# Kernel tuning notes

Measured on AMD Instinct MI355X. Metric: run time of the kernel, lower is better.

Reference implementation:

```python
import jax, jax.numpy as jnp
import numpy as np

B, N, C = 2, 8192, 768
H, K = 12, 256
D = C // H
HID = 4 * C
EPS = 1e-6

def layer_norm(x, w, b):
    mu = jnp.mean(x, axis=-1, keepdims=True)
    var = jnp.mean(jnp.square(x - mu), axis=-1, keepdims=True)
    return (x - mu) * jax.lax.rsqrt(var + EPS) * w + b

def setup_inputs() -> dict:
    key = jax.random.key(0)
    ks = jax.random.split(key, 8)
    s = 0.02
    return {
        "x": jax.random.normal(ks[0], (B, N, C), jnp.float32),
        "ln1_w": jnp.ones((C,), jnp.float32),
        "ln1_b": jnp.zeros((C,), jnp.float32),
        "qkv_w": jax.random.normal(ks[1], (C, 3 * C), jnp.float32) * s,
        "qkv_b": jnp.zeros((3 * C,), jnp.float32),
        "Ek": jax.random.normal(ks[2], (N, K), jnp.float32) * s,
        "Ev": jax.random.normal(ks[3], (N, K), jnp.float32) * s,
        "proj_w": jax.random.normal(ks[4], (C, C), jnp.float32) * s,
        "proj_b": jnp.zeros((C,), jnp.float32),
        "ln2_w": jnp.ones((C,), jnp.float32),
        "ln2_b": jnp.zeros((C,), jnp.float32),
        "fc1_w": jax.random.normal(ks[5], (C, HID), jnp.float32) * s,
        "fc1_b": jnp.zeros((HID,), jnp.float32),
        "fc2_w": jax.random.normal(ks[6], (HID, C), jnp.float32) * s,
        "fc2_b": jnp.zeros((C,), jnp.float32),
    }

def reference(x, ln1_w, ln1_b, qkv_w, qkv_b, Ek, Ev, proj_w, proj_b,
              ln2_w, ln2_b, fc1_w, fc1_b, fc2_w, fc2_b):
    scale = D ** -0.5
    # --- attention branch ---
    h = layer_norm(x, ln1_w, ln1_b)
    qkv = h @ qkv_w + qkv_b                      # (B,N,3C)
    qkv = qkv.reshape(B, N, 3, H, D).transpose(2, 0, 3, 1, 4)  # (3,B,H,N,D)
    q, k, v = qkv[0], qkv[1], qkv[2]
    # Linformer: project K/V along sequence dim N -> K
    k_proj = jnp.einsum('bhnd,nk->bhkd', k, Ek)
    v_proj = jnp.einsum('bhnd,nk->bhkd', v, Ev)
    logits = jnp.einsum('bhnd,bhkd->bhnk', q, k_proj) * scale
    logits = jnp.clip(logits, -50.0, 50.0)
    attn = jax.nn.softmax(logits, axis=-1)
    o = jnp.einsum('bhnk,bhkd->bhnd', attn, v_proj)
    o = o.transpose(0, 2, 1, 3).reshape(B, N, C)
    o = o @ proj_w + proj_b
    x = x + o                                    # alpha_attn = 1.0
    # --- MLP branch ---
    h = layer_norm(x, ln2_w, ln2_b)
    h = jax.nn.gelu(h @ fc1_w + fc1_b, approximate=False)
    h = h @ fc2_w + fc2_b
    return x + h                                 # alpha_mlp = 1.0
```

## Files before the change

kernel.cpp:

```cpp
#include <hip/hip_runtime.h>
#include <cstdint>

#define DEV __device__ __forceinline__

typedef __bf16 bf16x8 __attribute__((ext_vector_type(8)));
typedef float f32x4 __attribute__((ext_vector_type(4)));

DEV uint16_t f2bf(float f) {
  uint32_t u = __float_as_uint(f);
  u += 0x7FFFu + ((u >> 16) & 1u);
  return (uint16_t)(u >> 16);
}
DEV float bf2f(uint16_t h) { return __uint_as_float(((uint32_t)h) << 16); }

DEV void gload16(const void* g, void* l) {
  __builtin_amdgcn_global_load_lds((const __attribute__((address_space(1))) void*)g,
                                   (__attribute__((address_space(3))) void*)l, 16, 0, 0);
}

template <int N> DEV void waitcnt_vm() {
  if constexpr (N == 0) asm volatile("s_waitcnt vmcnt(0)" ::: "memory");
  else if constexpr (N == 3) asm volatile("s_waitcnt vmcnt(3)" ::: "memory");
  else if constexpr (N == 4) asm volatile("s_waitcnt vmcnt(4)" ::: "memory");
  else static_assert(N == 0 || N == 3 || N == 4, "unsupported vmcnt");
}

__global__ __launch_bounds__(256) void ln768(const float* __restrict__ x,
                                             const float* __restrict__ w,
                                             const float* __restrict__ b,
                                             uint16_t* __restrict__ out) {
  const size_t row = blockIdx.x;
  const float* xr = x + row * 768;
  const int t = threadIdx.x;
  float v0 = xr[t], v1 = xr[t + 256], v2 = xr[t + 512];
  float s = v0 + v1 + v2;
  float s2 = v0 * v0 + v1 * v1 + v2 * v2;
#pragma unroll
  for (int o = 32; o; o >>= 1) {
    s += __shfl_down(s, o);
    s2 += __shfl_down(s2, o);
  }
  __shared__ float sh[8];
  if ((t & 63) == 0) { sh[t >> 6] = s; sh[4 + (t >> 6)] = s2; }
  __syncthreads();
  s = sh[0] + sh[1] + sh[2] + sh[3];
  s2 = sh[4] + sh[5] + sh[6] + sh[7];
  const float mu = s * (1.f / 768.f);
  const float var = s2 * (1.f / 768.f) - mu * mu;
  const float rstd = rsqrtf(var + 1e-6f);
  uint16_t* orow = out + row * 768;
  orow[t]       = f2bf((v0 - mu) * rstd * w[t] + b[t]);
  orow[t + 256] = f2bf((v1 - mu) * rstd * w[t + 256] + b[t + 256]);
  orow[t + 512] = f2bf((v2 - mu) * rstd * w[t + 512] + b[t + 512]);
}

__global__ __launch_bounds__(256) void transpose_f2b(const float* __restrict__ in,
                                                     uint16_t* __restrict__ outp,
                                                     int ldin, int ldout) {
  __shared__ float tile[32][33];
  const int tx = threadIdx.x, ty = threadIdx.y;
  const size_t x = (size_t)blockIdx.x * 32 + tx;
  const size_t y = (size_t)blockIdx.y * 32 + ty;
#pragma unroll
  for (int j = 0; j < 4; ++j) tile[ty + j * 8][tx] = in[(y + j * 8) * ldin + x];
  __syncthreads();
  const size_t x2 = (size_t)blockIdx.y * 32 + tx;
  const size_t y2 = (size_t)blockIdx.x * 32 + ty;
#pragma unroll
  for (int j = 0; j < 4; ++j) outp[(y2 + j * 8) * ldout + x2] = f2bf(tile[tx][ty + j * 8]);
}

__global__ __launch_bounds__(256) void transpose_b2b(const uint16_t* __restrict__ in,
                                                     uint16_t* __restrict__ outp,
                                                     int ldin, int ldout) {
  __shared__ uint16_t tile[32][33];
  const int tx = threadIdx.x, ty = threadIdx.y;
  const size_t x = (size_t)blockIdx.x * 32 + tx;
  const size_t y = (size_t)blockIdx.y * 32 + ty;
#pragma unroll
  for (int j = 0; j < 4; ++j) tile[ty + j * 8][tx] = in[(y + j * 8) * ldin + x];
  __syncthreads();
  const size_t x2 = (size_t)blockIdx.y * 32 + tx;
  const size_t y2 = (size_t)blockIdx.x * 32 + ty;
#pragma unroll
  for (int j = 0; j < 4; ++j) outp[(y2 + j * 8) * ldout + x2] = tile[tx][ty + j * 8];
}

template <int BM, int BN, bool OUTBF, bool HASBIAS, bool DOGELU, bool HASRES>
__global__ __launch_bounds__(256) void gemm_nt(
    const uint16_t* __restrict__ Abase, const uint16_t* __restrict__ Bbase,
    void* __restrict__ Cbase, const float* __restrict__ bias,
    const float* __restrict__ resbase, int Kd, int lda, int ldb, int ldc,
    int zdiv, size_t sAhi, size_t sAlo, size_t sBhi, size_t sBlo,
    size_t sChi, size_t sClo) {
  const int z = blockIdx.z;
  const int zhi = z / zdiv, zlo = z - zhi * zdiv;
  const uint16_t* A = Abase + zhi * sAhi + zlo * sAlo;
  const uint16_t* B = Bbase + zhi * sBhi + zlo * sBlo;
  const size_t coff = zhi * sChi + zlo * sClo;

  constexpr int WTM = BM / 2, WTN = BN / 2;
  constexpr int FM = WTM / 16, FN = WTN / 16;
  const int tid = threadIdx.x;
  const int wave = tid >> 6, lane = tid & 63;
  const int wm = wave >> 1, wn = wave & 1;
  const int l16 = lane & 15, lhi = lane >> 4;

  __shared__ __align__(16) uint16_t sA[BM * 32];
  __shared__ __align__(16) uint16_t sB[BN * 32];

  f32x4 acc[FM][FN];
#pragma unroll
  for (int m = 0; m < FM; ++m)
#pragma unroll
    for (int n = 0; n < FN; ++n) acc[m][n] = f32x4{0.f, 0.f, 0.f, 0.f};

  const int row0 = blockIdx.x * BM;
  const int col0 = blockIdx.y * BN;
  const int rr = tid >> 2, cq = tid & 3;

  for (int k0 = 0; k0 < Kd; k0 += 32) {
    __syncthreads();
#pragma unroll
    for (int is = 0; is < BM / 64; ++is) {
      const uint16_t* g = A + (size_t)(row0 + is * 64 + rr) * lda + k0 + cq * 8;
      gload16(g, &sA[is * 2048 + tid * 8]);
    }
#pragma unroll
    for (int is = 0; is < BN / 64; ++is) {
      const uint16_t* g = B + (size_t)(col0 + is * 64 + rr) * ldb + k0 + cq * 8;
      gload16(g, &sB[is * 2048 + tid * 8]);
    }
    __syncthreads();

    bf16x8 af[FM], bq[FN];
#pragma unroll
    for (int m = 0; m < FM; ++m)
      af[m] = *(const bf16x8*)(&sA[(wm * WTM + m * 16 + l16) * 32 + lhi * 8]);
#pragma unroll
    for (int n = 0; n < FN; ++n)
      bq[n] = *(const bf16x8*)(&sB[(wn * WTN + n * 16 + l16) * 32 + lhi * 8]);
#pragma unroll
    for (int m = 0; m < FM; ++m)
#pragma unroll
      for (int n = 0; n < FN; ++n)
        acc[m][n] = __builtin_amdgcn_mfma_f32_16x16x32_bf16(af[m], bq[n], acc[m][n], 0, 0, 0);
  }

  float* Cf = (float*)Cbase;
  uint16_t* Cb = (uint16_t*)Cbase;
#pragma unroll
  for (int m = 0; m < FM; ++m) {
#pragma unroll
    for (int n = 0; n < FN; ++n) {
      const int col = col0 + wn * WTN + n * 16 + l16;
      float bv = 0.f;
      if (HASBIAS) bv = bias[col];
#pragma unroll
      for (int r = 0; r < 4; ++r) {
        const int row = row0 + wm * WTM + m * 16 + lhi * 4 + r;
        float v = acc[m][n][r];
        if (HASBIAS) v += bv;
        if (DOGELU) v = 0.5f * v * (1.f + erff(v * 0.70710678118654752f));
        const size_t cidx = coff + (size_t)row * ldc + col;
        if (HASRES) v += resbase[cidx];
        if (OUTBF) Cb[cidx] = f2bf(v);
        else Cf[cidx] = v;
      }
    }
  }
}

__global__ __launch_bounds__(256) void kv_reduce(const float* __restrict__ part,
                                                 uint16_t* __restrict__ kproj,
                                                 uint16_t* __restrict__ vprojT) {
  const int kvb = blockIdx.y;
  const int i = blockIdx.x * 256 + threadIdx.x;
  const float* p = part + (size_t)kvb * 8 * 196608 + i;
  float s = 0.f;
#pragma unroll
  for (int j = 0; j < 8; ++j) s += p[(size_t)j * 196608];
  const uint16_t v = f2bf(s);
  kproj[(size_t)kvb * 196608 + i] = v;
  if (kvb >= 2) {
    const int b = kvb - 2, k = i / 768, c = i % 768;
    vprojT[((size_t)(b * 768 + c)) * 256 + k] = v;
  }
}

__global__ __launch_bounds__(256, 3) void attn_fused(
    const uint16_t* __restrict__ qkv,
    const uint16_t* __restrict__ kproj,
    const uint16_t* __restrict__ vprojT,
    uint16_t* __restrict__ o) {
  const int bh = blockIdx.y;
  const int b = bh / 12, h = bh % 12;
  const int n0 = blockIdx.x * 64;
  const int tid = threadIdx.x, wave = tid >> 6, lane = tid & 63;
  const int l16 = lane & 15, lhi = lane >> 4;
  const int wm = wave >> 1, wn = wave & 1;

  __shared__ __align__(16) uint16_t sP[64 * 256];
  __shared__ float redm[2][64], reds[2][64], recs[64];

  const uint16_t* Kp = kproj + (size_t)b * 196608 + h * 64;
  const uint16_t* Qp = qkv + ((size_t)b * 8192 + n0) * 2304 + h * 64;
  const uint16_t* Vp = vprojT + ((size_t)b * 768 + h * 64) * 256;

  f32x4 st[8][2];
#pragma unroll
  for (int m = 0; m < 8; ++m)
#pragma unroll
    for (int nf = 0; nf < 2; ++nf) st[m][nf] = f32x4{0.f, 0.f, 0.f, 0.f};
#pragma unroll
  for (int ks = 0; ks < 2; ++ks) {
    bf16x8 kf[8], qf[2];
#pragma unroll
    for (int m = 0; m < 8; ++m) {
      const int kv = wm * 128 + m * 16 + l16;
      kf[m] = *(const bf16x8*)(Kp + (size_t)kv * 768 + ks * 32 + lhi * 8);
    }
#pragma unroll
    for (int nf = 0; nf < 2; ++nf) {
      const int n = wn * 32 + nf * 16 + l16;
      qf[nf] = *(const bf16x8*)(Qp + (size_t)n * 2304 + ks * 32 + lhi * 8);
    }
#pragma unroll
    for (int m = 0; m < 8; ++m)
#pragma unroll
      for (int nf = 0; nf < 2; ++nf)
        st[m][nf] = __builtin_amdgcn_mfma_f32_16x16x32_bf16(kf[m], qf[nf], st[m][nf], 0, 0, 0);
  }

  float pmax[2] = {-50.f, -50.f};
#pragma unroll
  for (int m = 0; m < 8; ++m)
#pragma unroll
    for (int nf = 0; nf < 2; ++nf)
#pragma unroll
      for (int r = 0; r < 4; ++r) {
        float v = fminf(fmaxf(st[m][nf][r] * 0.125f, -50.f), 50.f);
        st[m][nf][r] = v;
        pmax[nf] = fmaxf(pmax[nf], v);
      }
#pragma unroll
  for (int nf = 0; nf < 2; ++nf) {
    pmax[nf] = fmaxf(pmax[nf], __shfl_xor(pmax[nf], 16));
    pmax[nf] = fmaxf(pmax[nf], __shfl_xor(pmax[nf], 32));
  }
  if (lhi == 0) {
#pragma unroll
    for (int nf = 0; nf < 2; ++nf) redm[wm][wn * 32 + nf * 16 + l16] = pmax[nf];
  }
  __syncthreads();
  float M[2];
#pragma unroll
  for (int nf = 0; nf < 2; ++nf) {
    const int col = wn * 32 + nf * 16 + l16;
    M[nf] = fmaxf(redm[0][col], redm[1][col]);
  }

  float psum[2] = {0.f, 0.f};
#pragma unroll
  for (int m = 0; m < 8; ++m) {
#pragma unroll
    for (int nf = 0; nf < 2; ++nf) {
      float e0 = __expf(st[m][nf][0] - M[nf]);
      float e1 = __expf(st[m][nf][1] - M[nf]);
      float e2 = __expf(st[m][nf][2] - M[nf]);
      float e3 = __expf(st[m][nf][3] - M[nf]);
      psum[nf] += (e0 + e1) + (e2 + e3);
      uint2 pk;
      pk.x = (uint32_t)f2bf(e0) | ((uint32_t)f2bf(e1) << 16);
      pk.y = (uint32_t)f2bf(e2) | ((uint32_t)f2bf(e3) << 16);
      const int n = wn * 32 + nf * 16 + l16;
      const int kvb2 = (wm * 128 + m * 16 + lhi * 4) * 2;
      *(uint2*)((char*)sP + n * 512 + (kvb2 ^ ((n & 7) << 4))) = pk;
    }
  }
#pragma unroll
  for (int nf = 0; nf < 2; ++nf) {
    psum[nf] += __shfl_xor(psum[nf], 16);
    psum[nf] += __shfl_xor(psum[nf], 32);
  }
  if (lhi == 0) {
#pragma unroll
    for (int nf = 0; nf < 2; ++nf) reds[wm][wn * 32 + nf * 16 + l16] = psum[nf];
  }
  __syncthreads();
  if (wm == 0 && lhi == 0) {
#pragma unroll
    for (int nf = 0; nf < 2; ++nf) {
      const int col = wn * 32 + nf * 16 + l16;
      recs[col] = 1.f / (reds[0][col] + reds[1][col]);
    }
  }
  __syncthreads();

  f32x4 pacc[2][2];
#pragma unroll
  for (int mf = 0; mf < 2; ++mf)
#pragma unroll
    for (int nf = 0; nf < 2; ++nf) pacc[mf][nf] = f32x4{0.f, 0.f, 0.f, 0.f};
#pragma unroll
  for (int ks = 0; ks < 8; ++ks) {
    bf16x8 pa[2], vb[2];
#pragma unroll
    for (int mf = 0; mf < 2; ++mf) {
      const int n = wm * 32 + mf * 16 + l16;
      pa[mf] = *(const bf16x8*)((char*)sP + n * 512 + ((ks * 64 + lhi * 16) ^ ((n & 7) << 4)));
    }
#pragma unroll
    for (int nf = 0; nf < 2; ++nf) {
      const int d = wn * 32 + nf * 16 + l16;
      vb[nf] = *(const bf16x8*)(Vp + (size_t)d * 256 + ks * 32 + lhi * 8);
    }
#pragma unroll
    for (int mf = 0; mf < 2; ++mf)
#pragma unroll
      for (int nf = 0; nf < 2; ++nf)
        pacc[mf][nf] = __builtin_amdgcn_mfma_f32_16x16x32_bf16(pa[mf], vb[nf], pacc[mf][nf], 0, 0, 0);
  }
  uint16_t* orow = o + ((size_t)b * 8192 + n0) * 768 + h * 64;
#pragma unroll
  for (int mf = 0; mf < 2; ++mf) {
#pragma unroll
    for (int r = 0; r < 4; ++r) {
      const int n = wm * 32 + mf * 16 + lhi * 4 + r;
      const float inv = recs[n];
#pragma unroll
      for (int nf = 0; nf < 2; ++nf) {
        const int d = wn * 32 + nf * 16 + l16;
        orow[(size_t)n * 768 + d] = f2bf(pacc[mf][nf][r] * inv);
      }
    }
  }
}

template <int BM, int BN, int NTHR, int WGN, bool OUTBF, bool HASBIAS, bool DOGELU, bool HASRES>
__global__ __launch_bounds__(NTHR, (NTHR == 512) ? 4 : 3) void gemm8v2(
    const uint16_t* __restrict__ A, const uint16_t* __restrict__ B,
    void* __restrict__ Cbase, const float* __restrict__ bias,
    const float* __restrict__ res, int Kd, int lda, int ldb, int ldc) {
  constexpr int NWAVES = NTHR / 64;
  constexpr int WGM = NWAVES / WGN;
  constexpr int WROWS = BM / WGM, WCOLS = BN / WGN;
  constexpr int FM = WROWS / 16, FN = WCOLS / 16;
  constexpr int RPI = NTHR / 4;
  constexpr int IA = BM / RPI, IB = BN / RPI;
  constexpr int LPT = IA + IB;
  constexpr int ABUF = BM * 32, BBUF = BN * 32;
  __shared__ __align__(16) uint16_t lds[3 * (ABUF + BBUF)];

  const int nn = gridDim.y;
  const int nwg = gridDim.x * gridDim.y;
  const int bid = blockIdx.y * gridDim.x + blockIdx.x;
  const int q = nwg >> 3, r8 = nwg & 7, xcd = bid & 7, idx = bid >> 3;
  const int wg = (xcd < r8 ? xcd * (q + 1) : r8 * (q + 1) + (xcd - r8) * q) + idx;
  const int bm = wg / nn, bn = wg % nn;
  const int row0 = bm * BM, col0 = bn * BN;

  const int tid = threadIdx.x;
  const int wave = tid >> 6, lane = tid & 63;
  const int wm = wave / WGN, wn = wave % WGN;
  const int l16 = lane & 15, lhi = lane >> 4;
  const int srow = tid >> 2, sslot = tid & 3;

  auto stage = [&](int buf, int t) {
    const int k0 = t * 32;
    uint16_t* sa = lds + buf * (ABUF + BBUF);
    uint16_t* sb = sa + ABUF;
#pragma unroll
    for (int j = 0; j < IA; ++j) {
      const int rw = j * RPI + srow;
      const int sp = sslot ^ ((rw >> 1) & 3);
      gload16(A + (size_t)(row0 + rw) * lda + k0 + sp * 8, sa + rw * 32 + sslot * 8);
    }
#pragma unroll
    for (int j = 0; j < IB; ++j) {
      const int rw = j * RPI + srow;
      const int sp = sslot ^ ((rw >> 1) & 3);
      gload16(B + (size_t)(col0 + rw) * ldb + k0 + sp * 8, sb + rw * 32 + sslot * 8);
    }
  };

  f32x4 acc[FM][FN];
#pragma unroll
  for (int m = 0; m < FM; ++m)
#pragma unroll
    for (int n = 0; n < FN; ++n) acc[m][n] = f32x4{0.f, 0.f, 0.f, 0.f};

  const int NT = Kd >> 5;
  stage(0, 0);
  stage(1, 1);

  for (int t = 0; t < NT; ++t) {
    if (t < NT - 1) waitcnt_vm<LPT>();
    else waitcnt_vm<0>();
    __builtin_amdgcn_s_barrier();
    asm volatile("" ::: "memory");
    if (t + 2 < NT) stage((t + 2) % 3, t + 2);

    const uint16_t* sa = lds + (t % 3) * (ABUF + BBUF);
    const uint16_t* sb = sa + ABUF;
    bf16x8 af[FM], bf[FN];
#pragma unroll
    for (int n = 0; n < FN; ++n) {
      const int rw = wn * WCOLS + n * 16 + l16;
      bf[n] = *(const bf16x8*)(sb + rw * 32 + (lhi ^ ((rw >> 1) & 3)) * 8);
    }
#pragma unroll
    for (int m = 0; m < FM; ++m) {
      const int rw = wm * WROWS + m * 16 + l16;
      af[m] = *(const bf16x8*)(sa + rw * 32 + (lhi ^ ((rw >> 1) & 3)) * 8);
    }
    __builtin_amdgcn_s_setprio(1);
#pragma unroll
    for (int m = 0; m < FM; ++m)
#pragma unroll
      for (int n = 0; n < FN; ++n)
        acc[m][n] = __builtin_amdgcn_mfma_f32_16x16x32_bf16(af[m], bf[n], acc[m][n], 0, 0, 0);
    __builtin_amdgcn_s_setprio(0);
  }

  float* Cf = (float*)Cbase;
  uint16_t* Cb = (uint16_t*)Cbase;
#pragma unroll
  for (int m = 0; m < FM; ++m) {
#pragma unroll
    for (int n = 0; n < FN; ++n) {
      const int col = col0 + wn * WCOLS + n * 16 + l16;
      float bv = 0.f;
      if (HASBIAS) bv = bias[col];
#pragma unroll
      for (int r = 0; r < 4; ++r) {
        const int row = row0 + wm * WROWS + m * 16 + lhi * 4 + r;
        float v = acc[m][n][r] + bv;
        if (DOGELU) v = 0.5f * v * (1.f + erff(v * 0.70710678118654752f));
        const size_t cidx = (size_t)row * ldc + col;
        if (HASRES) v += res[cidx];
        if (OUTBF) Cb[cidx] = f2bf(v);
        else Cf[cidx] = v;
      }
    }
  }
}

extern "C" void kernel_launch(void* const* d_in, const int* in_sizes, int n_in,
                              void* d_out, int out_size, void* d_ws, size_t ws_size,
                              hipStream_t stream) {
  const float* x      = (const float*)d_in[0];
  const float* ln1_w  = (const float*)d_in[1];
  const float* ln1_b  = (const float*)d_in[2];
  const float* qkv_w  = (const float*)d_in[3];
  const float* qkv_b  = (const float*)d_in[4];
  const float* Ek     = (const float*)d_in[5];
  const float* Ev     = (const float*)d_in[6];
  const float* proj_w = (const float*)d_in[7];
  const float* proj_b = (const float*)d_in[8];
  const float* ln2_w  = (const float*)d_in[9];
  const float* ln2_b  = (const float*)d_in[10];
  const float* fc1_w  = (const float*)d_in[11];
  const float* fc1_b  = (const float*)d_in[12];
  const float* fc2_w  = (const float*)d_in[13];
  const float* fc2_b  = (const float*)d_in[14];
  float* out = (float*)d_out;

  char* w8 = (char*)d_ws;
  size_t off = 0;
  auto take = [&](size_t bytes) { char* p = w8 + off; off += bytes; return p; };
  uint16_t* qkv_wT  = (uint16_t*)take(2304ull * 768 * 2);
  uint16_t* proj_wT = (uint16_t*)take(768ull * 768 * 2);
  uint16_t* fc1_wT  = (uint16_t*)take(3072ull * 768 * 2);
  uint16_t* fc2_wT  = (uint16_t*)take(768ull * 3072 * 2);
  uint16_t* EkT     = (uint16_t*)take(256ull * 8192 * 2);
  uint16_t* EvT     = (uint16_t*)take(256ull * 8192 * 2);
  uint16_t* h_bf    = (uint16_t*)take(16384ull * 768 * 2);
  uint16_t* qkv_bf  = (uint16_t*)take(16384ull * 2304 * 2);
  uint16_t* big     = (uint16_t*)take(100663296ull);
  uint16_t* kproj   = (uint16_t*)take(2ull * 2 * 256 * 768 * 2);
  uint16_t* vprojT  = (uint16_t*)take(2ull * 768 * 256 * 2);
  uint16_t* o_bf    = (uint16_t*)take(16384ull * 768 * 2);
  float* part = (float*)o_bf;
  (void)ws_size; (void)in_sizes; (void)n_in; (void)out_size;

  const dim3 tb(32, 8);
  transpose_f2b<<<dim3(72, 24), tb, 0, stream>>>(qkv_w, qkv_wT, 2304, 768);
  transpose_f2b<<<dim3(24, 24), tb, 0, stream>>>(proj_w, proj_wT, 768, 768);
  transpose_f2b<<<dim3(96, 24), tb, 0, stream>>>(fc1_w, fc1_wT, 3072, 768);
  transpose_f2b<<<dim3(24, 96), tb, 0, stream>>>(fc2_w, fc2_wT, 768, 3072);
  transpose_f2b<<<dim3(8, 256), tb, 0, stream>>>(Ek, EkT, 256, 8192);
  transpose_f2b<<<dim3(8, 256), tb, 0, stream>>>(Ev, EvT, 256, 8192);
  ln768<<<16384, 256, 0, stream>>>(x, ln1_w, ln1_b, h_bf);
  gemm8v2<256, 128, 512, 2, true, true, false, false><<<dim3(64, 18), 512, 0, stream>>>(
      h_bf, qkv_wT, qkv_bf, qkv_b, nullptr, 768, 768, 768, 2304);
  uint16_t* kvT = big;
  for (int b = 0; b < 2; ++b) {
    transpose_b2b<<<dim3(24, 256), tb, 0, stream>>>(
        qkv_bf + (size_t)b * 8192 * 2304 + 768, kvT + (size_t)b * 768 * 8192, 2304, 8192);
    transpose_b2b<<<dim3(24, 256), tb, 0, stream>>>(
        qkv_bf + (size_t)b * 8192 * 2304 + 1536, kvT + (size_t)(2 + b) * 768 * 8192, 2304, 8192);
  }
  for (int kvb = 0; kvb < 4; ++kvb) {
    const uint16_t* Ab = (kvb < 2) ? EkT : EvT;
    gemm_nt<64, 64, false, false, false, false><<<dim3(4, 12, 8), 256, 0, stream>>>(
        Ab, kvT + (size_t)kvb * 768 * 8192, part + (size_t)kvb * 8 * 196608,
        nullptr, nullptr, 1024, 8192, 8192, 768,
        1, 1024, 0, 1024, 0, 196608, 0);
  }
  kv_reduce<<<dim3(768, 4), 256, 0, stream>>>(part, kproj, vprojT);
  attn_fused<<<dim3(128, 24), 256, 0, stream>>>(qkv_bf, kproj, vprojT, o_bf);
  gemm8v2<128, 128, 256, 2, false, true, false, true><<<dim3(128, 6), 256, 0, stream>>>(
      o_bf, proj_wT, out, proj_b, x, 768, 768, 768, 768);
  ln768<<<16384, 256, 0, stream>>>(out, ln2_w, ln2_b, h_bf);
  gemm8v2<256, 128, 512, 2, true, true, true, false><<<dim3(64, 24), 512, 0, stream>>>(
      h_bf, fc1_wT, big, fc1_b, nullptr, 768, 768, 768, 3072);
  gemm8v2<128, 128, 256, 2, false, true, false, true><<<dim3(128, 6), 256, 0, stream>>>(
      big, fc2_wT, out, fc2_b, out, 3072, 3072, 3072, 768);
}
```

Before: 534.4 us.

## Rework GEMM to BK=64 split prefetch, fuse KV projection, use tanh GELU

The GEMM kernel now uses 64-wide K tiles with 8-way XOR swizzling. It issues its prefetch in two halves interleaved with the MFMA phases and always runs 8 waves. The Linformer K/V projection no longer transposes the full K/V activations; a new kv_tn kernel reads strided columns of qkv directly, splits N into 4 chunks and leaves a 4-way reduction. Only the small projected V is transposed afterward. The exact erf GELU is replaced with a tanh-style approximation using exp, which removes erf cost but changes numerics slightly.

```diff
diff --git a/kernel.cpp b/kernel.cpp
--- a/kernel.cpp
+++ b/kernel.cpp
@@ -20,9 +20,14 @@
 
 template <int N> DEV void waitcnt_vm() {
   if constexpr (N == 0) asm volatile("s_waitcnt vmcnt(0)" ::: "memory");
-  else if constexpr (N == 3) asm volatile("s_waitcnt vmcnt(3)" ::: "memory");
   else if constexpr (N == 4) asm volatile("s_waitcnt vmcnt(4)" ::: "memory");
-  else static_assert(N == 0 || N == 3 || N == 4, "unsupported vmcnt");
+  else if constexpr (N == 6) asm volatile("s_waitcnt vmcnt(6)" ::: "memory");
+  else static_assert(N == 0 || N == 4 || N == 6, "unsupported vmcnt");
+}
+
+DEV float gelu_f(float v) {
+  float u = v * (0.7978845608f + 0.0356774081f * v * v);
+  return v / (1.f + __expf(-2.f * u));
 }
 
 __global__ __launch_bounds__(256) void ln768(const float* __restrict__ x,
@@ -86,106 +91,72 @@
   for (int j = 0; j < 4; ++j) outp[(y2 + j * 8) * ldout + x2] = tile[tx][ty + j * 8];
 }
 
-template <int BM, int BN, bool OUTBF, bool HASBIAS, bool DOGELU, bool HASRES>
-__global__ __launch_bounds__(256) void gemm_nt(
-    const uint16_t* __restrict__ Abase, const uint16_t* __restrict__ Bbase,
-    void* __restrict__ Cbase, const float* __restrict__ bias,
-    const float* __restrict__ resbase, int Kd, int lda, int ldb, int ldc,
-    int zdiv, size_t sAhi, size_t sAlo, size_t sBhi, size_t sBlo,
-    size_t sChi, size_t sClo) {
-  const int z = blockIdx.z;
-  const int zhi = z / zdiv, zlo = z - zhi * zdiv;
-  const uint16_t* A = Abase + zhi * sAhi + zlo * sAlo;
-  const uint16_t* B = Bbase + zhi * sBhi + zlo * sBlo;
-  const size_t coff = zhi * sChi + zlo * sClo;
-
-  constexpr int WTM = BM / 2, WTN = BN / 2;
-  constexpr int FM = WTM / 16, FN = WTN / 16;
-  const int tid = threadIdx.x;
-  const int wave = tid >> 6, lane = tid & 63;
+__global__ __launch_bounds__(256) void kv_tn(const uint16_t* __restrict__ EkT,
+                                             const uint16_t* __restrict__ EvT,
+                                             const uint16_t* __restrict__ qkv,
+                                             float* __restrict__ part) {
+  const int bid = blockIdx.x;
+  const int wg = (bid & 7) * 96 + (bid >> 3);
+  const int inner = wg & 15;
+  const int kt = inner & 3, ns = inner >> 2;
+  const int rest = wg >> 4;
+  const int ct = rest % 12, kvb = rest / 12;
+  const int kv = kvb >> 1, b = kvb & 1;
+  const int k0 = kt * 64, c0 = ct * 64, nsb = ns * 2048;
+
+  const uint16_t* E = kv ? EvT : EkT;
+  const uint16_t* KV = qkv + (size_t)b * 8192 * 2304 + 768 + kv * 768 + c0;
+  const int tid = threadIdx.x, wave = tid >> 6, lane = tid & 63;
+  const int l16 = lane & 15, lhi = lane >> 4;
   const int wm = wave >> 1, wn = wave & 1;
-  const int l16 = lane & 15, lhi = lane >> 4;
-
-  __shared__ __align__(16) uint16_t sA[BM * 32];
-  __shared__ __align__(16) uint16_t sB[BN * 32];
-
-  f32x4 acc[FM][FN];
-#pragma unroll
-  for (int m = 0; m < FM; ++m)
-#pragma unroll
-    for (int n = 0; n < FN; ++n) acc[m][n] = f32x4{0.f, 0.f, 0.f, 0.f};
-
-  const int row0 = blockIdx.x * BM;
-  const int col0 = blockIdx.y * BN;
-  const int rr = tid >> 2, cq = tid & 3;
-
-  for (int k0 = 0; k0 < Kd; k0 += 32) {
-    __syncthreads();
-#pragma unroll
-    for (int is = 0; is < BM / 64; ++is) {
-      const uint16_t* g = A + (size_t)(row0 + is * 64 + rr) * lda + k0 + cq * 8;
-      gload16(g, &sA[is * 2048 + tid * 8]);
-    }
-#pragma unroll
-    for (int is = 0; is < BN / 64; ++is) {
-      const uint16_t* g = B + (size_t)(col0 + is * 64 + rr) * ldb + k0 + cq * 8;
-      gload16(g, &sB[is * 2048 + tid * 8]);
-    }
-    __syncthreads();
-
-    bf16x8 af[FM], bq[FN];
-#pragma unroll
-    for (int m = 0; m < FM; ++m)
-      af[m] = *(const bf16x8*)(&sA[(wm * WTM + m * 16 + l16) * 32 + lhi * 8]);
-#pragma unroll
-    for (int n = 0; n < FN; ++n)
-      bq[n] = *(const bf16x8*)(&sB[(wn * WTN + n * 16 + l16) * 32 + lhi * 8]);
-#pragma unroll
-    for (int m = 0; m < FM; ++m)
-#pragma unroll
-      for (int n = 0; n < FN; ++n)
-        acc[m][n] = __builtin_amdgcn_mfma_f32_16x16x32_bf16(af[m], bq[n], acc[m][n], 0, 0, 0);
-  }
-
-  float* Cf = (float*)Cbase;
-  uint16_t* Cb = (uint16_t*)Cbase;
-#pragma unroll
-  for (int m = 0; m < FM; ++m) {
-#pragma unroll
-    for (int n = 0; n < FN; ++n) {
-      const int col = col0 + wn * WTN + n * 16 + l16;
-      float bv = 0.f;
-      if (HASBIAS) bv = bias[col];
-#pragma unroll
-      for (int r = 0; r < 4; ++r) {
-        const int row = row0 + wm * WTM + m * 16 + lhi * 4 + r;
-        float v = acc[m][n][r];
-        if (HASBIAS) v += bv;
-        if (DOGELU) v = 0.5f * v * (1.f + erff(v * 0.70710678118654752f));
-        const size_t cidx = coff + (size_t)row * ldc + col;
-        if (HASRES) v += resbase[cidx];
-        if (OUTBF) Cb[cidx] = f2bf(v);
-        else Cf[cidx] = v;
-      }
-    }
-  }
+
+  f32x4 acc[2][2];
+#pragma unroll
+  for (int m = 0; m < 2; ++m)
+#pragma unroll
+    for (int n = 0; n < 2; ++n) acc[m][n] = f32x4{0.f, 0.f, 0.f, 0.f};
+
+  const uint16_t* Eb = E + (size_t)(k0 + wm * 32 + l16) * 8192 + nsb + lhi * 8;
+  const uint16_t* KVb = KV + ((size_t)nsb + lhi * 8) * 2304 + wn * 32 + l16;
+
+  for (int n0 = 0; n0 < 2048; n0 += 32) {
+    bf16x8 ef[2];
+    ef[0] = *(const bf16x8*)(Eb + n0);
+    ef[1] = *(const bf16x8*)(Eb + 16 * 8192 + n0);
+    bf16x8 vf[2];
+#pragma unroll
+    for (int nf = 0; nf < 2; ++nf) {
+      const uint16_t* p = KVb + (size_t)n0 * 2304 + nf * 16;
+      union { bf16x8 v; uint16_t u[8]; } tu;
+#pragma unroll
+      for (int j = 0; j < 8; ++j) tu.u[j] = p[(size_t)j * 2304];
+      vf[nf] = tu.v;
+    }
+#pragma unroll
+    for (int m = 0; m < 2; ++m)
+#pragma unroll
+      for (int nf = 0; nf < 2; ++nf)
+        acc[m][nf] = __builtin_amdgcn_mfma_f32_16x16x32_bf16(ef[m], vf[nf], acc[m][nf], 0, 0, 0);
+  }
+
+  float* outp = part + ((size_t)ns * 4 + kvb) * 196608;
+#pragma unroll
+  for (int m = 0; m < 2; ++m)
+#pragma unroll
+    for (int nf = 0; nf < 2; ++nf)
+#pragma unroll
+      for (int r = 0; r < 4; ++r)
+        outp[(size_t)(k0 + wm * 32 + m * 16 + lhi * 4 + r) * 768 + c0 + wn * 32 + nf * 16 + l16] =
+            acc[m][nf][r];
 }
 
 __global__ __launch_bounds__(256) void kv_reduce(const float* __restrict__ part,
-                                                 uint16_t* __restrict__ kproj,
-                                                 uint16_t* __restrict__ vprojT) {
+                                                 uint16_t* __restrict__ kproj) {
   const int kvb = blockIdx.y;
   const int i = blockIdx.x * 256 + threadIdx.x;
-  const float* p = part + (size_t)kvb * 8 * 196608 + i;
-  float s = 0.f;
-#pragma unroll
-  for (int j = 0; j < 8; ++j) s += p[(size_t)j * 196608];
-  const uint16_t v = f2bf(s);
-  kproj[(size_t)kvb * 196608 + i] = v;
-  if (kvb >= 2) {
-    const int b = kvb - 2, k = i / 768, c = i % 768;
-    vprojT[((size_t)(b * 768 + c)) * 256 + k] = v;
-  }
+  const float* p = part + (size_t)kvb * 196608 + i;
+  float s = p[0] + p[786432] + p[2 * 786432] + p[3 * 786432];
+  kproj[(size_t)kvb * 196608 + i] = f2bf(s);
 }
 
 __global__ __launch_bounds__(256, 3) void attn_fused(
@@ -217,8 +188,8 @@
     bf16x8 kf[8], qf[2];
 #pragma unroll
     for (int m = 0; m < 8; ++m) {
-      const int kv = wm * 128 + m * 16 + l16;
-      kf[m] = *(const bf16x8*)(Kp + (size_t)kv * 768 + ks * 32 + lhi * 8);
+      const int kvi = wm * 128 + m * 16 + l16;
+      kf[m] = *(const bf16x8*)(Kp + (size_t)kvi * 768 + ks * 32 + lhi * 8);
     }
 #pragma unroll
     for (int nf = 0; nf < 2; ++nf) {
@@ -337,19 +308,16 @@
   }
 }
 
-template <int BM, int BN, int NTHR, int WGN, bool OUTBF, bool HASBIAS, bool DOGELU, bool HASRES>
-__global__ __launch_bounds__(NTHR, (NTHR == 512) ? 4 : 3) void gemm8v2(
+template <int BM, int BN, bool OUTBF, bool HASBIAS, bool DOGELU, bool HASRES>
+__global__ __launch_bounds__(512, 2) void gemm3(
     const uint16_t* __restrict__ A, const uint16_t* __restrict__ B,
     void* __restrict__ Cbase, const float* __restrict__ bias,
     const float* __restrict__ res, int Kd, int lda, int ldb, int ldc) {
-  constexpr int NWAVES = NTHR / 64;
-  constexpr int WGM = NWAVES / WGN;
-  constexpr int WROWS = BM / WGM, WCOLS = BN / WGN;
+  constexpr int WROWS = BM / 4, WCOLS = BN / 2;
   constexpr int FM = WROWS / 16, FN = WCOLS / 16;
-  constexpr int RPI = NTHR / 4;
-  constexpr int IA = BM / RPI, IB = BN / RPI;
+  constexpr int IA = BM / 64, IB = BN / 64;
   constexpr int LPT = IA + IB;
-  constexpr int ABUF = BM * 32, BBUF = BN * 32;
+  constexpr int ABUF = BM * 64, BBUF = BN * 64;
   __shared__ __align__(16) uint16_t lds[3 * (ABUF + BBUF)];
 
   const int nn = gridDim.y;
@@ -362,27 +330,20 @@
 
   const int tid = threadIdx.x;
   const int wave = tid >> 6, lane = tid & 63;
-  const int wm = wave / WGN, wn = wave % WGN;
+  const int wm = wave >> 1, wn = wave & 1;
   const int l16 = lane & 15, lhi = lane >> 4;
-  const int srow = tid >> 2, sslot = tid & 3;
-
-  auto stage = [&](int buf, int t) {
-    const int k0 = t * 32;
-    uint16_t* sa = lds + buf * (ABUF + BBUF);
-    uint16_t* sb = sa + ABUF;
-#pragma unroll
-    for (int j = 0; j < IA; ++j) {
-      const int rw = j * RPI + srow;
-      const int sp = sslot ^ ((rw >> 1) & 3);
-      gload16(A + (size_t)(row0 + rw) * lda + k0 + sp * 8, sa + rw * 32 + sslot * 8);
-    }
-#pragma unroll
-    for (int j = 0; j < IB; ++j) {
-      const int rw = j * RPI + srow;
-      const int sp = sslot ^ ((rw >> 1) & 3);
-      gload16(B + (size_t)(col0 + rw) * ldb + k0 + sp * 8, sb + rw * 32 + sslot * 8);
-    }
+  const int srow = tid >> 3, sslot = tid & 7;
+
+  auto stageA = [&](uint16_t* sa, int k0, int j) {
+    const int rw = j * 64 + srow;
+    const int sp = sslot ^ (rw & 7);
+    gload16(A + (size_t)(row0 + rw) * lda + k0 + sp * 8, sa + rw * 64 + sslot * 8);
   };
+  auto stageB = [&](uint16_t* sb, int k0, int j) {
+    const int rw = j * 64 + srow;
+    const int sp = sslot ^ (rw & 7);
+    gload16(B + (size_t)(col0 + rw) * ldb + k0 + sp * 8, sb + rw * 64 + sslot * 8);
+  };
 
   f32x4 acc[FM][FN];
 #pragma unroll
@@ -390,37 +351,80 @@
 #pragma unroll
     for (int n = 0; n < FN; ++n) acc[m][n] = f32x4{0.f, 0.f, 0.f, 0.f};
 
-  const int NT = Kd >> 5;
-  stage(0, 0);
-  stage(1, 1);
+  const int NT = Kd >> 6;
+#pragma unroll
+  for (int j = 0; j < IA; ++j) stageA(lds, 0, j);
+#pragma unroll
+  for (int j = 0; j < IB; ++j) stageB(lds + ABUF, 0, j);
+#pragma unroll
+  for (int j = 0; j < IA; ++j) stageA(lds + (ABUF + BBUF), 64, j);
+#pragma unroll
+  for (int j = 0; j < IB; ++j) stageB(lds + (ABUF + BBUF) + ABUF, 64, j);
 
   for (int t = 0; t < NT; ++t) {
     if (t < NT - 1) waitcnt_vm<LPT>();
     else waitcnt_vm<0>();
     __builtin_amdgcn_s_barrier();
     asm volatile("" ::: "memory");
-    if (t + 2 < NT) stage((t + 2) % 3, t + 2);
-
     const uint16_t* sa = lds + (t % 3) * (ABUF + BBUF);
     const uint16_t* sb = sa + ABUF;
-    bf16x8 af[FM], bf[FN];
-#pragma unroll
-    for (int n = 0; n < FN; ++n) {
-      const int rw = wn * WCOLS + n * 16 + l16;
-      bf[n] = *(const bf16x8*)(sb + rw * 32 + (lhi ^ ((rw >> 1) & 3)) * 8);
-    }
-#pragma unroll
-    for (int m = 0; m < FM; ++m) {
-      const int rw = wm * WROWS + m * 16 + l16;
-      af[m] = *(const bf16x8*)(sa + rw * 32 + (lhi ^ ((rw >> 1) & 3)) * 8);
-    }
-    __builtin_amdgcn_s_setprio(1);
-#pragma unroll
-    for (int m = 0; m < FM; ++m)
-#pragma unroll
-      for (int n = 0; n < FN; ++n)
-        acc[m][n] = __builtin_amdgcn_mfma_f32_16x16x32_bf16(af[m], bf[n], acc[m][n], 0, 0, 0);
-    __builtin_amdgcn_s_setprio(0);
+    uint16_t* pa = lds + ((t + 2) % 3) * (ABUF + BBUF);
+    uint16_t* pb = pa + ABUF;
+    const bool pf = (t + 2) < NT;
+    const int k0p = (t + 2) * 64;
+
+    if (pf) {
+#pragma unroll
+      for (int j = 0; j < IA / 2; ++j) stageA(pa, k0p, j);
+#pragma unroll
+      for (int j = 0; j < IB / 2; ++j) stageB(pb, k0p, j);
+    }
+    {
+      bf16x8 af[FM], bfr[FN];
+#pragma unroll
+      for (int n = 0; n < FN; ++n) {
+        const int rw = wn * WCOLS + n * 16 + l16;
+        bfr[n] = *(const bf16x8*)(sb + rw * 64 + ((lhi) ^ (rw & 7)) * 8);
+      }
+#pragma unroll
+      for (int m = 0; m < FM; ++m) {
+        const int rw = wm * WROWS + m * 16 + l16;
+        af[m] = *(const bf16x8*)(sa + rw * 64 + ((lhi) ^ (rw & 7)) * 8);
+      }
+      __builtin_amdgcn_s_setprio(1);
+#pragma unroll
+      for (int m = 0; m < FM; ++m)
+#pragma unroll
+        for (int n = 0; n < FN; ++n)
+          acc[m][n] = __builtin_amdgcn_mfma_f32_16x16x32_bf16(af[m], bfr[n], acc[m][n], 0, 0, 0);
+      __builtin_amdgcn_s_setprio(0);
+    }
+    if (pf) {
+#pragma unroll
+      for (int j = IA / 2; j < IA; ++j) stageA(pa, k0p, j);
+#pragma unroll
+      for (int j = IB / 2; j < IB; ++j) stageB(pb, k0p, j);
+    }
+    {
+      bf16x8 af[FM], bfr[FN];
+#pragma unroll
+      for (int n = 0; n < FN; ++n) {
+        const int rw = wn * WCOLS + n * 16 + l16;
+        bfr[n] = *(const bf16x8*)(sb + rw * 64 + ((4 + lhi) ^ (rw & 7)) * 8);
+      }
+#pragma unroll
+      for (int m = 0; m < FM; ++m) {
+        const int rw = wm * WROWS + m * 16 + l16;
+        af[m] = *(const bf16x8*)(sa + rw * 64 + ((4 + lhi) ^ (rw & 7)) * 8);
+      }
+      __builtin_amdgcn_s_setprio(1);
+#pragma unroll
+      for (int m = 0; m < FM; ++m)
+#pragma unroll
+        for (int n = 0; n < FN; ++n)
+          acc[m][n] = __builtin_amdgcn_mfma_f32_16x16x32_bf16(af[m], bfr[n], acc[m][n], 0, 0, 0);
+      __builtin_amdgcn_s_setprio(0);
+    }
   }
 
   float* Cf = (float*)Cbase;
@@ -436,7 +440,7 @@
       for (int r = 0; r < 4; ++r) {
         const int row = row0 + wm * WROWS + m * 16 + lhi * 4 + r;
         float v = acc[m][n][r] + bv;
-        if (DOGELU) v = 0.5f * v * (1.f + erff(v * 0.70710678118654752f));
+        if (DOGELU) v = gelu_f(v);
         const size_t cidx = (size_t)row * ldc + col;
         if (HASRES) v += res[cidx];
         if (OUTBF) Cb[cidx] = f2bf(v);
@@ -481,7 +485,7 @@
   uint16_t* kproj   = (uint16_t*)take(2ull * 2 * 256 * 768 * 2);
   uint16_t* vprojT  = (uint16_t*)take(2ull * 768 * 256 * 2);
   uint16_t* o_bf    = (uint16_t*)take(16384ull * 768 * 2);
-  float* part = (float*)o_bf;
+  float* part = (float*)big;
   (void)ws_size; (void)in_sizes; (void)n_in; (void)out_size;
 
   const dim3 tb(32, 8);
@@ -492,29 +496,19 @@
   transpose_f2b<<<dim3(8, 256), tb, 0, stream>>>(Ek, EkT, 256, 8192);
   transpose_f2b<<<dim3(8, 256), tb, 0, stream>>>(Ev, EvT, 256, 8192);
   ln768<<<16384, 256, 0, stream>>>(x, ln1_w, ln1_b, h_bf);
-  gemm8v2<256, 128, 512, 2, true, true, false, false><<<dim3(64, 18), 512, 0, stream>>>(
+  gemm3<256, 128, true, true, false, false><<<dim3(64, 18), 512, 0, stream>>>(
       h_bf, qkv_wT, qkv_bf, qkv_b, nullptr, 768, 768, 768, 2304);
-  uint16_t* kvT = big;
-  for (int b = 0; b < 2; ++b) {
-    transpose_b2b<<<dim3(24, 256), tb, 0, stream>>>(
-        qkv_bf + (size_t)b * 8192 * 2304 + 768, kvT + (size_t)b * 768 * 8192, 2304, 8192);
-    transpose_b2b<<<dim3(24, 256), tb, 0, stream>>>(
-        qkv_bf + (size_t)b * 8192 * 2304 + 1536, kvT + (size_t)(2 + b) * 768 * 8192, 2304, 8192);
-  }
-  for (int kvb = 0; kvb < 4; ++kvb) {
-    const uint16_t* Ab = (kvb < 2) ? EkT : EvT;
-    gemm_nt<64, 64, false, false, false, false><<<dim3(4, 12, 8), 256, 0, stream>>>(
-        Ab, kvT + (size_t)kvb * 768 * 8192, part + (size_t)kvb * 8 * 196608,
-        nullptr, nullptr, 1024, 8192, 8192, 768,
-        1, 1024, 0, 1024, 0, 196608, 0);
-  }
-  kv_reduce<<<dim3(768, 4), 256, 0, stream>>>(part, kproj, vprojT);
+  kv_tn<<<768, 256, 0, stream>>>(EkT, EvT, qkv_bf, part);
+  kv_reduce<<<dim3(768, 4), 256, 0, stream>>>(part, kproj);
+  for (int b = 0; b < 2; ++b)
+    transpose_b2b<<<dim3(24, 8), tb, 0, stream>>>(
+        kproj + (size_t)(2 + b) * 196608, vprojT + (size_t)b * 768 * 256, 768, 256);
   attn_fused<<<dim3(128, 24), 256, 0, stream>>>(qkv_bf, kproj, vprojT, o_bf);
-  gemm8v2<128, 128, 256, 2, false, true, false, true><<<dim3(128, 6), 256, 0, stream>>>(
+  gemm3<128, 128, false, true, false, true><<<dim3(128, 6), 512, 0, stream>>>(
       o_bf, proj_wT, out, proj_b, x, 768, 768, 768, 768);
   ln768<<<16384, 256, 0, stream>>>(out, ln2_w, ln2_b, h_bf);
-  gemm8v2<256, 128, 512, 2, true, true, true, false><<<dim3(64, 24), 512, 0, stream>>>(
+  gemm3<256, 128, true, true, true, false><<<dim3(64, 24), 512, 0, stream>>>(
       h_bf, fc1_wT, big, fc1_b, nullptr, 768, 768, 768, 3072);
-  gemm8v2<128, 128, 256, 2, false, true, false, true><<<dim3(128, 6), 256, 0, stream>>>(
+  gemm3<128, 128, false, true, false, true><<<dim3(128, 6), 512, 0, stream>>>(
       big, fc2_wT, out, fc2_b, out, 3072, 3072, 3072, 768);
 }
```

After: 489.9 us. 8.3% less time.
